# Kernel tuning notes

Hardware: AMD Instinct MI355X
Metric: run time of the kernel (lower is better)

## Reference

```python
import jax, jax.numpy as jnp
import numpy as np
from jax import lax

B, C_IN, C_OUT, H, W, E = 16, 256, 256, 32, 32, 8


def setup_inputs() -> dict:
    key = jax.random.key(0)
    k = jax.random.split(key, 5)
    x = jax.random.normal(k[0], (B, C_IN, H, W), dtype=jnp.float32)
    # router: Conv2d(C_IN, E, kernel_size=1) -> weight [E, C_IN], bias [E]
    wc = jax.random.normal(k[1], (E, C_IN), dtype=jnp.float32) / np.sqrt(C_IN)
    bc = jnp.zeros((E,), dtype=jnp.float32)
    # experts: E x Conv2d(C_IN, C_OUT, 3, padding=1) + ReLU
    we = jax.random.normal(k[2], (E, C_OUT, C_IN, 3, 3), dtype=jnp.float32) / np.sqrt(C_IN * 9)
    be = jnp.zeros((E, C_OUT), dtype=jnp.float32)
    return {"x": x, "wc": wc, "bc": bc, "we": we, "be": be}


def reference(x, wc, bc, we, be):
    Bx = x.shape[0]
    # controller: 1x1 conv then global avg-pool == pool then linear
    pooled = jnp.mean(x, axis=(2, 3))                      # [B, C_IN]
    logits = pooled @ wc.T + bc                            # [B, E]
    decisions = jnp.argmax(logits, axis=1)                 # [B] int
    # run ALL experts on the full batch as one grouped conv: weight [E*C_OUT, C_IN, 3, 3]
    w_all = we.reshape(E * C_OUT, C_IN, 3, 3)
    y = lax.conv_general_dilated(
        x, w_all, window_strides=(1, 1), padding="SAME",
        dimension_numbers=("NCHW", "OIHW", "NCHW"))        # [B, E*C_OUT, H, W]
    y = y + be.reshape(1, E * C_OUT, 1, 1)
    y = jax.nn.relu(y).reshape(Bx, E, C_OUT, H, W)
    # faithful to forward_test: out block i is components[dec[i]](x) for the FULL batch
    # out[i*B + j] = y[j, dec[i]]
    gathered = y[:, decisions]                             # [j, i, C_OUT, H, W]
    out = jnp.swapaxes(gathered, 0, 1).reshape(Bx * Bx, C_OUT, H, W)
    return out
```

## Files before the change

### kernel.cpp

```cpp
#include <hip/hip_runtime.h>
#include <hip/hip_bf16.h>
#include <stdint.h>

#define B_    16
#define CIN   256
#define COUT  256
#define E_    8
#define HW    1024
#define PH    34
#define PW    34

typedef __attribute__((ext_vector_type(8))) short  short8;
typedef __attribute__((ext_vector_type(4))) float  floatx4;

#define XT_OFF 17408
#define XT_BYTES (B_*PH*PW*CIN*2)
#define WT_OFF (XT_OFF + XT_BYTES)

__device__ __forceinline__ void gld_lds16(const void* g, void* l) {
    __builtin_amdgcn_global_load_lds(
        (const __attribute__((address_space(1))) unsigned int*)g,
        (__attribute__((address_space(3))) unsigned int*)l,
        16, 0, 0);
}

__global__ void xpose_kernel(const float* __restrict__ x, unsigned short* __restrict__ xt,
                             float* __restrict__ pooled) {
    int b = blockIdx.x;
    int hw0 = blockIdx.y * 32;
    int ci0 = blockIdx.z * 32;
    __shared__ float tile[32][33];
    int t = threadIdx.x;
    int j = t & 31;
    int i = t >> 5;
    #pragma unroll
    for (int p = 0; p < 4; ++p)
        tile[i + p*8][j] = x[((size_t)b*CIN + ci0 + i + p*8)*HW + hw0 + j];
    __syncthreads();
    if (t < 32) {
        float s = 0.0f;
        #pragma unroll
        for (int q = 0; q < 32; ++q) s += tile[t][q];
        atomicAdd(&pooled[b*CIN + ci0 + t], s);
    }
    if (t < 128) {
        int g = t & 3;
        int hwl = t >> 2;
        int hw = hw0 + hwl;
        int h = hw >> 5, w = hw & 31;
        short8 v;
        #pragma unroll
        for (int q = 0; q < 8; ++q) {
            __hip_bfloat16 hv = __float2bfloat16(tile[g*8 + q][hwl]);
            v[q] = *(short*)&hv;
        }
        *(short8*)&xt[(((size_t)b*PH + h + 1)*PW + (w + 1))*CIN + ci0 + g*8] = v;
    }
}

__global__ void decide_kernel(const float* __restrict__ pooled, const float* __restrict__ wc,
                              const float* __restrict__ bc, int* __restrict__ dec) {
    int t = threadIdx.x;
    int b = t >> 3, e = t & 7;
    float acc = 0.0f;
    const float4* pp = (const float4*)(pooled + b*CIN);
    const float4* ww = (const float4*)(wc + e*CIN);
    #pragma unroll 4
    for (int i = 0; i < CIN/4; ++i) {
        float4 p = pp[i], w = ww[i];
        acc += p.x*w.x + p.y*w.y + p.z*w.z + p.w*w.w;
    }
    acc = acc * (1.0f/1024.0f) + bc[e];
    __shared__ float lg[16][8];
    lg[b][e] = acc;
    __syncthreads();
    if (e == 0) {
        float best = lg[b][0]; int bi = 0;
        #pragma unroll
        for (int j = 1; j < 8; ++j) { if (lg[b][j] > best) { best = lg[b][j]; bi = j; } }
        dec[b] = bi;
    }
}

__global__ void wpose_kernel(const float* __restrict__ we, unsigned short* __restrict__ wt) {
    int e = blockIdx.x >> 8, co = blockIdx.x & 255;
    __shared__ float buf[CIN*9];
    const float* src = we + ((size_t)e*COUT + co)*CIN*9;
    int t = threadIdx.x;
    #pragma unroll
    for (int k = 0; k < 9; ++k) buf[t + k*256] = src[t + k*256];
    __syncthreads();
    for (int idx = t; idx < 288; idx += 256) {
        int rs = idx >> 5, grp = idx & 31;
        short8 v;
        #pragma unroll
        for (int q = 0; q < 8; ++q) {
            __hip_bfloat16 h = __float2bfloat16(buf[(grp*8 + q)*9 + rs]);
            v[q] = *(short*)&h;
        }
        *(short8*)&wt[(((size_t)e*9 + rs)*COUT + co)*CIN + grp*8] = v;
    }
}

__global__ __launch_bounds__(256, 4) void conv_kernel(
    const unsigned short* __restrict__ xt, const unsigned short* __restrict__ wt,
    const float* __restrict__ be, const int* __restrict__ dec,
    float* __restrict__ out) {

    int tile = blockIdx.x;
    int b = blockIdx.y;
    int e = blockIdx.z;
    int mt = tile >> 3, nt = tile & 7;

    int dcs[16];
    #pragma unroll
    for (int i = 0; i < 16; ++i) dcs[i] = dec[i];
    bool active = false;
    #pragma unroll
    for (int i = 0; i < 16; ++i) active |= (dcs[i] == e);
    if (!active) return;

    __shared__ __align__(16) unsigned short sA[3][512*8];
    __shared__ __align__(16) unsigned short sB[816*8];

    int t = threadIdx.x;
    int wave = t >> 6, lane = t & 63;
    int wm = wave >> 1, wn = wave & 1;
    int kg = lane >> 4, ln = lane & 15;

    int ph0 = nt * 4;
    int co0 = mt * 128;

    floatx4 acc[4][4];
    #pragma unroll
    for (int i = 0; i < 4; ++i)
        #pragma unroll
        for (int j = 0; j < 4; ++j) acc[i][j] = (floatx4)0.0f;

    const unsigned short* xb = xt + ((size_t)b*PH + ph0)*PW*CIN;
    const unsigned short* wb = wt + (size_t)e*9*COUT*CIN + (size_t)co0*CIN;

    auto stageA = [&](int ck, int sh, int buf) {
        const unsigned short* wsrc = wb + (size_t)sh*COUT*CIN + ck*32;
        #pragma unroll
        for (int k = 0; k < 2; ++k) {
            int c = t + k*256;
            int row = c >> 2, gs = c & 3;
            int g = gs ^ ((row >> 1) & 3);
            gld_lds16(wsrc + (size_t)row*CIN + g*8, &sA[buf][c*8]);
        }
    };
    auto stageB = [&](int ck) {
        const unsigned short* xsrc = xb + ck*32;
        #pragma unroll
        for (int k = 0; k < 3; ++k) {
            int c = t + k*256;
            int rB = c >> 2, gs = c & 3;
            int g = gs ^ ((rB >> 1) & 3);
            gld_lds16(xsrc + (size_t)rB*CIN + g*8, &sB[c*8]);
        }
        if (t < 64) {
            int c = t + 768;
            int cc = c < 816 ? c : 815;
            int rB = cc >> 2, gs = cc & 3;
            int g = gs ^ ((rB >> 1) & 3);
            if (c < 816) gld_lds16(xsrc + (size_t)rB*CIN + g*8, &sB[c*8]);
            else         gld_lds16(xsrc + (size_t)rB*CIN + g*8, &sB[815*8]);
        }
    };

    stageB(0);
    stageA(0, 0, 0);
    stageA(0, 1, 1);
    asm volatile("s_waitcnt vmcnt(2)" ::: "memory");
    __builtin_amdgcn_s_barrier();

    for (int ck = 0; ck < 8; ++ck) {
        for (int sh = 0; sh < 9; ++sh) {
            int it = ck*9 + sh;
            int ab = it % 3;
            int r = sh / 3, s = sh - r*3;
            bool doA = (it + 2 < 72);

            short8 a[4], bv[4];
            auto readA = [&]() {
                #pragma unroll
                for (int im = 0; im < 4; ++im) {
                    int row = wm*64 + im*16 + ln;
                    int cL = row*4 + (kg ^ ((row >> 1) & 3));
                    a[im] = *(const short8*)(&sA[ab][cL*8]);
                }
            };
            auto readB = [&]() {
                #pragma unroll
                for (int in = 0; in < 4; ++in) {
                    int n  = wn*64 + in*16 + ln;
                    int hl = n >> 5, wl = n & 31;
                    int rB = (hl + r)*34 + (wl + s);
                    int cL = rB*4 + (kg ^ ((rB >> 1) & 3));
                    bv[in] = *(const short8*)(&sB[cL*8]);
                }
            };

            if (sh == 8 && ck < 7) {
                readB();
                asm volatile("s_waitcnt lgkmcnt(0)" ::: "memory");
                __builtin_amdgcn_s_barrier();
                stageB(ck + 1);
                { int nit = it + 2; int nck = nit/9; stageA(nck, nit - nck*9, nit % 3); }
                readA();
            } else {
                if (doA) { int nit = it + 2; int nck = nit/9; stageA(nck, nit - nck*9, nit % 3); }
                readA();
                readB();
            }

            #pragma unroll
            for (int im = 0; im < 4; ++im)
                #pragma unroll
                for (int in = 0; in < 4; ++in)
                    acc[im][in] = __builtin_amdgcn_mfma_f32_16x16x32_bf16(bv[in], a[im], acc[im][in], 0, 0, 0);

            if (it != 71) {
                if (doA) asm volatile("s_waitcnt vmcnt(2) lgkmcnt(0)" ::: "memory");
                else     asm volatile("s_waitcnt vmcnt(0) lgkmcnt(0)" ::: "memory");
                __builtin_amdgcn_s_barrier();
            }
        }
    }

    float bias[4];
    #pragma unroll
    for (int im = 0; im < 4; ++im)
        bias[im] = be[e*COUT + co0 + wm*64 + im*16 + ln];
    #pragma unroll
    for (int im = 0; im < 4; ++im)
        #pragma unroll
        for (int in = 0; in < 4; ++in)
            #pragma unroll
            for (int rg = 0; rg < 4; ++rg) {
                float v = acc[im][in][rg] + bias[im];
                acc[im][in][rg] = v > 0.0f ? v : 0.0f;
            }

    for (int i = 0; i < 16; ++i) {
        if (dcs[i] != e) continue;
        float* ob = out + (size_t)(i*16 + b)*COUT*HW;
        #pragma unroll
        for (int im = 0; im < 4; ++im) {
            int co = co0 + wm*64 + im*16 + ln;
            float* orow = ob + (size_t)co*HW + nt*128 + wn*64 + kg*4;
            #pragma unroll
            for (int in = 0; in < 4; ++in)
                *(floatx4*)(orow + in*16) = acc[im][in];
        }
    }
}

extern "C" void kernel_launch(void* const* d_in, const int* in_sizes, int n_in,
                              void* d_out, int out_size, void* d_ws, size_t ws_size,
                              hipStream_t stream) {
    const float* x  = (const float*)d_in[0];
    const float* wc = (const float*)d_in[1];
    const float* bc = (const float*)d_in[2];
    const float* we = (const float*)d_in[3];
    const float* be = (const float*)d_in[4];
    float* out = (float*)d_out;

    char* ws = (char*)d_ws;
    int*   dec    = (int*)ws;
    float* pooled = (float*)(ws + 64);
    unsigned short* xt = (unsigned short*)(ws + XT_OFF);
    unsigned short* wt = (unsigned short*)(ws + WT_OFF);

    hipMemsetAsync(ws, 0, XT_OFF + XT_BYTES, stream);

    xpose_kernel <<<dim3(16, 32, 8), 256, 0, stream>>>(x, xt, pooled);
    wpose_kernel <<<2048, 256, 0, stream>>>(we, wt);
    decide_kernel<<<1, 128, 0, stream>>>(pooled, wc, bc, dec);
    conv_kernel  <<<dim3(16, 16, 8), 256, 0, stream>>>(xt, wt, be, dec, out);
}
```

Measured before the change: 491.4 us.

## Enlarge conv tile to 128x256 with double-buffered input staging

Each block now computes 128 output channels by 256 pixels (8 rows) instead of 128x128. Each wave covers all 128 channels and 64 pixels with a 4x8 accumulator array, which raises weight reuse per LDS load and halves the grid. The input halo tile is double-buffered and prefetched one shift early, so the mid-chunk barrier that stalled to restage B is gone. MFMA sections are wrapped in setprio. The cost is more accumulator registers (launch bounds drop to 2 blocks per SIMD), more LDS and fewer blocks, which lowers occupancy.

```diff
diff --git a/kernel.cpp b/kernel.cpp
--- a/kernel.cpp
+++ b/kernel.cpp
@@ -102,40 +102,38 @@
     }
 }
 
-__global__ __launch_bounds__(256, 4) void conv_kernel(
+__global__ __launch_bounds__(256, 2) void conv_kernel(
     const unsigned short* __restrict__ xt, const unsigned short* __restrict__ wt,
     const float* __restrict__ be, const int* __restrict__ dec,
     float* __restrict__ out) {
 
-    int tile = blockIdx.x;
+    int mt = blockIdx.x >> 2, ht = blockIdx.x & 3;
     int b = blockIdx.y;
     int e = blockIdx.z;
-    int mt = tile >> 3, nt = tile & 7;
-
-    int dcs[16];
-    #pragma unroll
-    for (int i = 0; i < 16; ++i) dcs[i] = dec[i];
+
     bool active = false;
-    #pragma unroll
-    for (int i = 0; i < 16; ++i) active |= (dcs[i] == e);
+    {
+        const volatile int* dv = (const volatile int*)dec;
+        #pragma unroll
+        for (int i = 0; i < 16; ++i) active |= (dv[i] == e);
+    }
     if (!active) return;
 
     __shared__ __align__(16) unsigned short sA[3][512*8];
-    __shared__ __align__(16) unsigned short sB[816*8];
-
-    int t = threadIdx.x;
-    int wave = t >> 6, lane = t & 63;
-    int wm = wave >> 1, wn = wave & 1;
+    __shared__ __align__(16) unsigned short sB[2][1536*8];
+
+    int t = threadIdx.x;
+    int w = t >> 6, lane = t & 63;
     int kg = lane >> 4, ln = lane & 15;
 
-    int ph0 = nt * 4;
+    int ph0 = ht * 8;
     int co0 = mt * 128;
 
-    floatx4 acc[4][4];
+    floatx4 acc[4][8];
     #pragma unroll
     for (int i = 0; i < 4; ++i)
         #pragma unroll
-        for (int j = 0; j < 4; ++j) acc[i][j] = (floatx4)0.0f;
+        for (int j = 0; j < 8; ++j) acc[i][j] = (floatx4)0.0f;
 
     const unsigned short* xb = xt + ((size_t)b*PH + ph0)*PW*CIN;
     const unsigned short* wb = wt + (size_t)e*9*COUT*CIN + (size_t)co0*CIN;
@@ -150,109 +148,94 @@
             gld_lds16(wsrc + (size_t)row*CIN + g*8, &sA[buf][c*8]);
         }
     };
-    auto stageB = [&](int ck) {
+    auto stageB = [&](int ck, int buf) {
         const unsigned short* xsrc = xb + ck*32;
         #pragma unroll
-        for (int k = 0; k < 3; ++k) {
+        for (int k = 0; k < 6; ++k) {
             int c = t + k*256;
-            int rB = c >> 2, gs = c & 3;
-            int g = gs ^ ((rB >> 1) & 3);
-            gld_lds16(xsrc + (size_t)rB*CIN + g*8, &sB[c*8]);
-        }
-        if (t < 64) {
-            int c = t + 768;
-            int cc = c < 816 ? c : 815;
+            int cc = c < 1360 ? c : 1359;
             int rB = cc >> 2, gs = cc & 3;
             int g = gs ^ ((rB >> 1) & 3);
-            if (c < 816) gld_lds16(xsrc + (size_t)rB*CIN + g*8, &sB[c*8]);
-            else         gld_lds16(xsrc + (size_t)rB*CIN + g*8, &sB[815*8]);
+            gld_lds16(xsrc + (size_t)rB*CIN + g*8, &sB[buf][c*8]);
         }
     };
 
-    stageB(0);
+    stageB(0, 0);
     stageA(0, 0, 0);
     stageA(0, 1, 1);
     asm volatile("s_waitcnt vmcnt(2)" ::: "memory");
     __builtin_amdgcn_s_barrier();
 
     for (int ck = 0; ck < 8; ++ck) {
+        int bb = ck & 1;
         for (int sh = 0; sh < 9; ++sh) {
             int it = ck*9 + sh;
             int ab = it % 3;
             int r = sh / 3, s = sh - r*3;
             bool doA = (it + 2 < 72);
-
-            short8 a[4], bv[4];
-            auto readA = [&]() {
-                #pragma unroll
-                for (int im = 0; im < 4; ++im) {
-                    int row = wm*64 + im*16 + ln;
-                    int cL = row*4 + (kg ^ ((row >> 1) & 3));
-                    a[im] = *(const short8*)(&sA[ab][cL*8]);
-                }
-            };
-            auto readB = [&]() {
-                #pragma unroll
-                for (int in = 0; in < 4; ++in) {
-                    int n  = wn*64 + in*16 + ln;
-                    int hl = n >> 5, wl = n & 31;
-                    int rB = (hl + r)*34 + (wl + s);
-                    int cL = rB*4 + (kg ^ ((rB >> 1) & 3));
-                    bv[in] = *(const short8*)(&sB[cL*8]);
-                }
-            };
-
-            if (sh == 8 && ck < 7) {
-                readB();
-                asm volatile("s_waitcnt lgkmcnt(0)" ::: "memory");
-                __builtin_amdgcn_s_barrier();
-                stageB(ck + 1);
-                { int nit = it + 2; int nck = nit/9; stageA(nck, nit - nck*9, nit % 3); }
-                readA();
-            } else {
-                if (doA) { int nit = it + 2; int nck = nit/9; stageA(nck, nit - nck*9, nit % 3); }
-                readA();
-                readB();
-            }
-
+            bool doB = (sh == 7) && (ck < 7);
+
+            if (doA) { int nit = it + 2; int nck = nit/9; stageA(nck, nit - nck*9, nit % 3); }
+            if (doB) stageB(ck + 1, bb ^ 1);
+
+            short8 a[8], bv[4];
+            #pragma unroll
+            for (int jn = 0; jn < 8; ++jn) {
+                int row = jn*16 + ln;
+                int cL = row*4 + (kg ^ ((row >> 1) & 3));
+                a[jn] = *(const short8*)(&sA[ab][cL*8]);
+            }
+            #pragma unroll
+            for (int im = 0; im < 4; ++im) {
+                int n  = w*64 + im*16 + ln;
+                int hl = n >> 5, wl = n & 31;
+                int rB = (hl + r)*34 + (wl + s);
+                int cL = rB*4 + (kg ^ ((rB >> 1) & 3));
+                bv[im] = *(const short8*)(&sB[bb][cL*8]);
+            }
+
+            __builtin_amdgcn_s_setprio(1);
             #pragma unroll
             for (int im = 0; im < 4; ++im)
                 #pragma unroll
-                for (int in = 0; in < 4; ++in)
-                    acc[im][in] = __builtin_amdgcn_mfma_f32_16x16x32_bf16(bv[in], a[im], acc[im][in], 0, 0, 0);
+                for (int jn = 0; jn < 8; ++jn)
+                    acc[im][jn] = __builtin_amdgcn_mfma_f32_16x16x32_bf16(bv[im], a[jn], acc[im][jn], 0, 0, 0);
+            __builtin_amdgcn_s_setprio(0);
 
             if (it != 71) {
-                if (doA) asm volatile("s_waitcnt vmcnt(2) lgkmcnt(0)" ::: "memory");
-                else     asm volatile("s_waitcnt vmcnt(0) lgkmcnt(0)" ::: "memory");
+                if (doB)      asm volatile("s_waitcnt vmcnt(8) lgkmcnt(0)" ::: "memory");
+                else if (doA) asm volatile("s_waitcnt vmcnt(2) lgkmcnt(0)" ::: "memory");
+                else          asm volatile("s_waitcnt vmcnt(0) lgkmcnt(0)" ::: "memory");
                 __builtin_amdgcn_s_barrier();
             }
         }
     }
 
-    float bias[4];
+    float bias[8];
+    #pragma unroll
+    for (int jn = 0; jn < 8; ++jn)
+        bias[jn] = be[e*COUT + co0 + jn*16 + ln];
     #pragma unroll
     for (int im = 0; im < 4; ++im)
-        bias[im] = be[e*COUT + co0 + wm*64 + im*16 + ln];
-    #pragma unroll
-    for (int im = 0; im < 4; ++im)
-        #pragma unroll
-        for (int in = 0; in < 4; ++in)
+        #pragma unroll
+        for (int jn = 0; jn < 8; ++jn)
             #pragma unroll
             for (int rg = 0; rg < 4; ++rg) {
-                float v = acc[im][in][rg] + bias[im];
-                acc[im][in][rg] = v > 0.0f ? v : 0.0f;
-            }
-
+                float v = acc[im][jn][rg] + bias[jn];
+                acc[im][jn][rg] = v > 0.0f ? v : 0.0f;
+            }
+
+    const volatile int* dv = (const volatile int*)dec;
     for (int i = 0; i < 16; ++i) {
-        if (dcs[i] != e) continue;
+        if (dv[i] != e) continue;
         float* ob = out + (size_t)(i*16 + b)*COUT*HW;
         #pragma unroll
-        for (int im = 0; im < 4; ++im) {
-            int co = co0 + wm*64 + im*16 + ln;
-            float* orow = ob + (size_t)co*HW + nt*128 + wn*64 + kg*4;
-            #pragma unroll
-            for (int in = 0; in < 4; ++in)
-                *(floatx4*)(orow + in*16) = acc[im][in];
+        for (int jn = 0; jn < 8; ++jn) {
+            int co = co0 + jn*16 + ln;
+            float* orow = ob + (size_t)co*HW + ht*256 + w*64 + kg*4;
+            #pragma unroll
+            for (int im = 0; im < 4; ++im)
+                *(floatx4*)(orow + im*16) = acc[im][jn];
         }
     }
 }
@@ -278,5 +261,5 @@
     xpose_kernel <<<dim3(16, 32, 8), 256, 0, stream>>>(x, xt, pooled);
     wpose_kernel <<<2048, 256, 0, stream>>>(we, wt);
     decide_kernel<<<1, 128, 0, stream>>>(pooled, wc, bc, dec);
-    conv_kernel  <<<dim3(16, 16, 8), 256, 0, stream>>>(xt, wt, be, dec, out);
-}
+    conv_kernel  <<<dim3(8, 16, 8), 256, 0, stream>>>(xt, wt, be, dec, out);
+}
```

Result: slower. 538.8 us (+9.6%).
